# Optimization experiments

Measured on AMD Instinct MI355X. Metric: run time of the kernel, lower is better.

Reference implementation:

```python
import jax, jax.numpy as jnp
import numpy as np

N = 100000       # nodes per graph
H = 384          # hidden_dim
GRID = 10 * 10 * 7   # flattened grid feature size (10x10 UV grid, 7 channels)
NTYPES = 6       # len(surface_type_map)
ENT = NTYPES + 1 # one-hot entity_types + scalar area


def setup_inputs() -> dict:
    key = jax.random.key(0)
    ks = jax.random.split(key, 16)
    f32 = jnp.float32
    d = {}
    d["x1"] = jax.random.normal(ks[0], (N, 10, 10, 7), dtype=f32)
    d["is_face1"] = jax.random.uniform(ks[1], (N,), dtype=f32)
    d["entity_types1"] = jax.random.randint(ks[2], (N,), 0, NTYPES)
    d["area1"] = jax.random.uniform(ks[3], (N,), dtype=f32)
    d["x2"] = jax.random.normal(ks[4], (N, 10, 10, 7), dtype=f32)
    d["is_face2"] = jax.random.uniform(ks[5], (N,), dtype=f32)
    d["entity_types2"] = jax.random.randint(ks[6], (N,), 0, NTYPES)
    d["area2"] = jax.random.uniform(ks[7], (N,), dtype=f32)
    # MLP params (num_layers=2: Linear -> ELU -> Linear), fan-in scaled init
    d["W1g"] = jax.random.normal(ks[8], (GRID, H), dtype=f32) / np.sqrt(GRID)
    d["b1g"] = jnp.zeros((H,), dtype=f32)
    d["W2g"] = jax.random.normal(ks[9], (H, H), dtype=f32) / np.sqrt(H)
    d["b2g"] = jnp.zeros((H,), dtype=f32)
    d["W1e"] = jax.random.normal(ks[10], (ENT, H), dtype=f32) / np.sqrt(ENT)
    d["b1e"] = jnp.zeros((H,), dtype=f32)
    d["W2e"] = jax.random.normal(ks[11], (H, H), dtype=f32) / np.sqrt(H)
    d["b2e"] = jnp.zeros((H,), dtype=f32)
    return d


def _embed_one(x, is_face, entity_types, area, W1g, b1g, W2g, b2g, W1e, b1e, W2e, b2e):
    n = x.shape[0]
    face_mask = is_face > 0.5                      # which nodes are B-rep faces
    grid = x.reshape(n, -1)                        # [n, 700], mlp path
    hg = jax.nn.elu(grid @ W1g + b1g) @ W2g + b2g  # grid branch MLP
    ent = jnp.concatenate(
        [jax.nn.one_hot(entity_types, NTYPES, dtype=x.dtype), area[:, None]], axis=1
    )                                              # [n, 7]
    he = jax.nn.elu(ent @ W1e + b1e) @ W2e + b2e   # entity branch MLP
    # gather->MLP->scatter-add into zeros == masked dense (no batchnorm, row-wise MLP)
    return jnp.where(face_mask[:, None], hg + he, jnp.zeros((), x.dtype))


def reference(x1, is_face1, entity_types1, area1, x2, is_face2, entity_types2, area2,
              W1g, b1g, W2g, b2g, W1e, b1e, W2e, b2e):
    o1 = _embed_one(x1, is_face1, entity_types1, area1, W1g, b1g, W2g, b2g, W1e, b1e, W2e, b2e)
    o2 = _embed_one(x2, is_face2, entity_types2, area2, W1g, b1g, W2g, b2g, W1e, b1e, W2e, b2e)
    return (o1, o2)
```

## Files before the change

kernel.cpp:

```cpp
#include <hip/hip_runtime.h>
#include <hip/hip_bf16.h>

typedef __attribute__((ext_vector_type(8))) short short8;
typedef __attribute__((ext_vector_type(4))) short svec4;
typedef __attribute__((ext_vector_type(8))) __bf16 bf16x8;
typedef __attribute__((ext_vector_type(4))) float f32x4;

#define NN 100000
#define HD 384
#define K1T 22
#define K2T 24
#define NBLK 98

#define OFF_B1  0
#define OFF_B2  540672
#define OFF_T   1130496
#define OFF_V   1139712
#define OFF_BI  1141248
#define OFF_IDX 1142784
#define OFF_CNT 1942784
#define OFF_OFFS 1943568
#define OFF_TOT 1944352

union Frag { short s[8]; bf16x8 v; };

__device__ __forceinline__ short f2bf(float f) {
  union { __bf16 h; short s; } u;
  u.h = (__bf16)f;
  return u.s;
}

__device__ __forceinline__ float elu(float v) {
  return v > 0.f ? v : __expf(v) - 1.f;
}

__global__ void prep_kernel(const float* __restrict__ W1g, const float* __restrict__ b1g,
                            const float* __restrict__ W2g, const float* __restrict__ b2g,
                            const float* __restrict__ W1e, const float* __restrict__ b1e,
                            const float* __restrict__ W2e, const float* __restrict__ b2e,
                            char* __restrict__ ws) {
  int t = blockIdx.x * 256 + threadIdx.x;
  short* B1 = (short*)(ws + OFF_B1);
  short* B2 = (short*)(ws + OFF_B2);
  float* Tt = (float*)(ws + OFF_T);
  float* Vt = (float*)(ws + OFF_V);
  float* Bi = (float*)(ws + OFF_BI);
  if (t < 33792) {
    int lane = t & 63, rest = t >> 6;
    int kt = rest % K1T, nt = rest / K1T;
    int col = nt * 16 + (lane & 15);
    int kb = kt * 32 + (lane >> 4) * 8;
    short8 v;
#pragma unroll
    for (int i = 0; i < 8; ++i) {
      int k = kb + i;
      v[i] = (k < 700) ? f2bf(W1g[k * 384 + col]) : (short)0;
    }
    *(short8*)(B1 + (size_t)t * 8) = v;
  } else if (t < 70656) {
    int t2 = t - 33792;
    int lane = t2 & 63, rest = t2 >> 6;
    int kt = rest % K2T, nt = rest / K2T;
    int col = nt * 16 + (lane & 15);
    int kb = kt * 32 + (lane >> 4) * 8;
    short8 v;
#pragma unroll
    for (int i = 0; i < 8; ++i) {
      int k = kb + i;
      v[i] = (k < 384) ? f2bf(W2g[k * 384 + col]) : f2bf(W2e[(k - 384) * 384 + col]);
    }
    *(short8*)(B2 + (size_t)t2 * 8) = v;
  } else if (t < 73728) {
    int r = t - 70656;
    int which = r / 384, c = r % 384;
    if (which < 6)       Tt[r] = W1e[which * 384 + c] + b1e[c];
    else if (which == 6) Vt[c] = W1e[6 * 384 + c];
    else                 Bi[c] = b2g[c] + b2e[c];
  }
}

__global__ void count_kernel(const float* __restrict__ isf1, const float* __restrict__ isf2,
                             char* __restrict__ ws) {
  int g = blockIdx.y;
  const float* isf = g ? isf2 : isf1;
  int i = blockIdx.x * 1024 + threadIdx.x;
  bool face = (i < NN) && (isf[i] > 0.5f);
  unsigned long long b = __ballot(face);
  __shared__ int wc[16];
  int lane = threadIdx.x & 63, wid = threadIdx.x >> 6;
  if (lane == 0) wc[wid] = __popcll(b);
  __syncthreads();
  if (threadIdx.x == 0) {
    int s = 0;
#pragma unroll
    for (int w = 0; w < 16; ++w) s += wc[w];
    ((int*)(ws + OFF_CNT))[g * NBLK + blockIdx.x] = s;
  }
}

__global__ void scan_kernel(char* __restrict__ ws) {
  int t = threadIdx.x;
  if (t < 2) {
    const int* cnt = (const int*)(ws + OFF_CNT) + t * NBLK;
    int* offs = (int*)(ws + OFF_OFFS) + t * NBLK;
    int* tot = (int*)(ws + OFF_TOT);
    int run = 0;
    for (int b = 0; b < NBLK; ++b) { offs[b] = run; run += cnt[b]; }
    tot[t] = run;
  }
}

__global__ void compact_kernel(const float* __restrict__ isf1, const float* __restrict__ isf2,
                               char* __restrict__ ws) {
  int g = blockIdx.y;
  const float* isf = g ? isf2 : isf1;
  const int* offs = (const int*)(ws + OFF_OFFS) + g * NBLK;
  int totF = ((const int*)(ws + OFF_TOT))[g];
  int* idx = (int*)(ws + OFF_IDX) + g * NN;
  int bx = blockIdx.x;
  int i = bx * 1024 + threadIdx.x;
  bool valid = i < NN;
  bool face = valid && (isf[i] > 0.5f);
  unsigned long long bf = __ballot(face);
  unsigned long long bv = __ballot(valid);
  int lane = threadIdx.x & 63, wid = threadIdx.x >> 6;
  __shared__ int wF[16], wV[16];
  if (lane == 0) { wF[wid] = __popcll(bf); wV[wid] = __popcll(bv); }
  __syncthreads();
  int baseF = 0, baseV = 0;
  for (int w = 0; w < wid; ++w) { baseF += wF[w]; baseV += wV[w]; }
  unsigned long long lmask = (1ull << lane) - 1ull;
  int pF = __popcll(bf & lmask);
  int pV = __popcll(bv & lmask);
  if (face) {
    idx[offs[bx] + baseF + pF] = i;
  } else if (valid) {
    int nfBefore = bx * 1024 - offs[bx];
    int nfIn = (baseV + pV) - (baseF + pF);
    idx[totF + nfBefore + nfIn] = i;
  }
}

__global__ __launch_bounds__(256, 3) void face_embed_kernel(
    const float* __restrict__ x1, const int* __restrict__ et1, const float* __restrict__ ar1,
    const float* __restrict__ x2, const int* __restrict__ et2, const float* __restrict__ ar2,
    const float* __restrict__ b1g, const char* __restrict__ ws,
    float* __restrict__ out) {
  const int g = blockIdx.y;
  const float* x = g ? x2 : x1;
  const int* et  = g ? et2 : et1;
  const float* ar = g ? ar2 : ar1;
  float* o = out + (size_t)g * NN * HD;
  const int* idx = (const int*)(ws + OFF_IDX) + g * NN;
  const int totF = ((const int*)(ws + OFF_TOT))[g];
  const int nFB = (totF + 31) >> 5;
  const int bx = blockIdx.x;
  const int tid = threadIdx.x;

  if (bx >= nFB) {
    int totN = NN - totF;
    int base = (bx - nFB) * 32;
    if (base >= totN) return;
    const int* idxN = idx + totF;
    f32x4 z = {0.f, 0.f, 0.f, 0.f};
#pragma unroll
    for (int it = 0; it < 12; ++it) {
      int c = tid + it * 256;
      int r = c / 96, cc = c % 96;
      if (base + r < totN) {
        int node = idxN[base + r];
        *(f32x4*)(o + (size_t)node * HD + cc * 4) = z;
      }
    }
    return;
  }

  __shared__ short As[32 * 704];
  __shared__ int sN[32];
  short* h1s = As;

  const bf16x8* B1 = (const bf16x8*)(ws + OFF_B1);
  const bf16x8* B2 = (const bf16x8*)(ws + OFF_B2);
  const float* Tg  = (const float*)(ws + OFF_T);
  const float* Vg  = (const float*)(ws + OFF_V);
  const float* Big = (const float*)(ws + OFF_BI);

  const int row0 = bx * 32;
  if (tid < 32) {
    sN[tid] = (row0 + tid < totF) ? idx[row0 + tid] : -1;
    int byte = (tid * 1408 + 1400) ^ ((tid & 7) << 4);
    *(unsigned long long*)((char*)As + byte) = 0ull;
  }
  __syncthreads();

#pragma unroll 4
  for (int it = 0; it < 22; ++it) {
    int c = tid + it * 256;
    if (c < 5600) {
      int r = c / 175, cc = c % 175;
      int node = sN[r];
      if (node >= 0) {
        f32x4 v = *(const f32x4*)(x + (size_t)node * 700 + cc * 4);
        svec4 p;
#pragma unroll
        for (int i = 0; i < 4; ++i) p[i] = f2bf(v[i]);
        int byte = (r * 1408 + cc * 8) ^ ((r & 7) << 4);
        *(svec4*)((char*)As + byte) = p;
      }
    }
  }

  const int wid = tid >> 6, lane = tid & 63;
  const int lr = lane & 15, gq = lane >> 4;

  float b1c[6], b2c[6];
#pragma unroll
  for (int n = 0; n < 6; ++n) {
    int col = (wid * 6 + n) * 16 + lr;
    b1c[n] = b1g[col];
    b2c[n] = Big[col];
  }
  __syncthreads();

  f32x4 acc[2][6] = {};
  for (int kt = 0; kt < K1T; ++kt) {
    Frag a[2];
#pragma unroll
    for (int m = 0; m < 2; ++m) {
      int row = m * 16 + lr;
      int byte = (row * 1408 + kt * 64 + gq * 16) ^ ((row & 7) << 4);
      a[m].v = *(const bf16x8*)((const char*)As + byte);
    }
#pragma unroll
    for (int n = 0; n < 6; ++n) {
      bf16x8 b = B1[((wid * 6 + n) * K1T + kt) * 64 + lane];
#pragma unroll
      for (int m = 0; m < 2; ++m)
        acc[m][n] = __builtin_amdgcn_mfma_f32_16x16x32_bf16(a[m].v, b, acc[m][n], 0, 0, 0);
    }
  }
  __syncthreads();

#pragma unroll
  for (int m = 0; m < 2; ++m)
#pragma unroll
    for (int n = 0; n < 6; ++n) {
      int col = (wid * 6 + n) * 16 + lr;
#pragma unroll
      for (int r2 = 0; r2 < 4; ++r2) {
        int row = m * 16 + 4 * gq + r2;
        float hv = elu(acc[m][n][r2] + b1c[n]);
        int byte = (row * 768 + col * 2) ^ ((row & 15) << 4);
        *(short*)((char*)h1s + byte) = f2bf(hv);
      }
    }
  __syncthreads();

  int nde[2]; float nda[2];
#pragma unroll
  for (int m = 0; m < 2; ++m) {
    int node = sN[m * 16 + lr];
    if (node >= 0) { nde[m] = et[node]; nda[m] = ar[node]; }
    else           { nde[m] = 0;        nda[m] = 0.f; }
  }

  f32x4 acc2[2][6] = {};
  for (int kt = 0; kt < K2T; ++kt) {
    Frag a[2];
    if (kt < 12) {
#pragma unroll
      for (int m = 0; m < 2; ++m) {
        int row = m * 16 + lr;
        int byte = (row * 768 + (kt * 32 + gq * 8) * 2) ^ ((row & 15) << 4);
        a[m].v = *(const bf16x8*)((const char*)h1s + byte);
      }
    } else {
      int c0 = (kt - 12) * 32 + gq * 8;
#pragma unroll
      for (int m = 0; m < 2; ++m) {
        const float* Tp = Tg + nde[m] * 384 + c0;
        const float* Vp = Vg + c0;
#pragma unroll
        for (int i = 0; i < 8; ++i)
          a[m].s[i] = f2bf(elu(Tp[i] + nda[m] * Vp[i]));
      }
    }
#pragma unroll
    for (int n = 0; n < 6; ++n) {
      bf16x8 b = B2[((wid * 6 + n) * K2T + kt) * 64 + lane];
#pragma unroll
      for (int m = 0; m < 2; ++m)
        acc2[m][n] = __builtin_amdgcn_mfma_f32_16x16x32_bf16(a[m].v, b, acc2[m][n], 0, 0, 0);
    }
  }

#pragma unroll
  for (int m = 0; m < 2; ++m) {
#pragma unroll
    for (int r2 = 0; r2 < 4; ++r2) {
      int node = sN[m * 16 + 4 * gq + r2];
      if (node >= 0) {
#pragma unroll
        for (int n = 0; n < 6; ++n) {
          int col = (wid * 6 + n) * 16 + lr;
          o[(size_t)node * HD + col] = acc2[m][n][r2] + b2c[n];
        }
      }
    }
  }
}

extern "C" void kernel_launch(void* const* d_in, const int* in_sizes, int n_in,
                              void* d_out, int out_size, void* d_ws, size_t ws_size,
                              hipStream_t stream) {
  (void)n_in; (void)out_size; (void)ws_size; (void)in_sizes;
  const float* x1  = (const float*)d_in[0];
  const float* is1 = (const float*)d_in[1];
  const int*   et1 = (const int*)d_in[2];
  const float* ar1 = (const float*)d_in[3];
  const float* x2  = (const float*)d_in[4];
  const float* is2 = (const float*)d_in[5];
  const int*   et2 = (const int*)d_in[6];
  const float* ar2 = (const float*)d_in[7];
  const float* W1g = (const float*)d_in[8];
  const float* b1g = (const float*)d_in[9];
  const float* W2g = (const float*)d_in[10];
  const float* b2g = (const float*)d_in[11];
  const float* W1e = (const float*)d_in[12];
  const float* b1e = (const float*)d_in[13];
  const float* W2e = (const float*)d_in[14];
  const float* b2e = (const float*)d_in[15];
  float* out = (float*)d_out;
  char* ws = (char*)d_ws;

  prep_kernel<<<dim3(288), dim3(256), 0, stream>>>(W1g, b1g, W2g, b2g, W1e, b1e, W2e, b2e, ws);
  count_kernel<<<dim3(NBLK, 2), dim3(1024), 0, stream>>>(is1, is2, ws);
  scan_kernel<<<dim3(1), dim3(64), 0, stream>>>(ws);
  compact_kernel<<<dim3(NBLK, 2), dim3(1024), 0, stream>>>(is1, is2, ws);

  dim3 grid(NN / 32 + 1, 2);
  face_embed_kernel<<<grid, dim3(256), 0, stream>>>(
      x1, et1, ar1, x2, et2, ar2, b1g, ws, out);
}
```

Before: 371.1 us.

## Load grid MFMA A-fragments directly from global, dropping LDS staging

The first GEMM no longer stages gathered x rows into shared memory. Each lane reads its A fragment straight from global memory, converts it to bf16 in registers, and zero-pads the tail of the 700-wide row. This removes the LDS tile, a staging loop and one barrier, shrinks shared memory (which may raise occupancy), and reuses one accumulator set for both GEMMs. In exchange, each wave issues redundant, less-coalesced global loads, and every wave re-reads the same A rows across its 6 column groups.

```diff
diff --git a/kernel.cpp b/kernel.cpp
--- a/kernel.cpp
+++ b/kernel.cpp
@@ -175,9 +175,8 @@
     return;
   }
 
-  __shared__ short As[32 * 704];
+  __shared__ short h1s[32 * 384];
   __shared__ int sN[32];
-  short* h1s = As;
 
   const bf16x8* B1 = (const bf16x8*)(ws + OFF_B1);
   const bf16x8* B2 = (const bf16x8*)(ws + OFF_B2);
@@ -186,29 +185,8 @@
   const float* Big = (const float*)(ws + OFF_BI);
 
   const int row0 = bx * 32;
-  if (tid < 32) {
-    sN[tid] = (row0 + tid < totF) ? idx[row0 + tid] : -1;
-    int byte = (tid * 1408 + 1400) ^ ((tid & 7) << 4);
-    *(unsigned long long*)((char*)As + byte) = 0ull;
-  }
+  if (tid < 32) sN[tid] = (row0 + tid < totF) ? idx[row0 + tid] : -1;
   __syncthreads();
-
-#pragma unroll 4
-  for (int it = 0; it < 22; ++it) {
-    int c = tid + it * 256;
-    if (c < 5600) {
-      int r = c / 175, cc = c % 175;
-      int node = sN[r];
-      if (node >= 0) {
-        f32x4 v = *(const f32x4*)(x + (size_t)node * 700 + cc * 4);
-        svec4 p;
-#pragma unroll
-        for (int i = 0; i < 4; ++i) p[i] = f2bf(v[i]);
-        int byte = (r * 1408 + cc * 8) ^ ((r & 7) << 4);
-        *(svec4*)((char*)As + byte) = p;
-      }
-    }
-  }
 
   const int wid = tid >> 6, lane = tid & 63;
   const int lr = lane & 15, gq = lane >> 4;
@@ -220,16 +198,30 @@
     b1c[n] = b1g[col];
     b2c[n] = Big[col];
   }
-  __syncthreads();
+  int nde[2]; float nda[2];
+  const float* xp[2];
+#pragma unroll
+  for (int m = 0; m < 2; ++m) {
+    int node = sN[m * 16 + lr];
+    if (node >= 0) { nde[m] = et[node]; nda[m] = ar[node]; }
+    else           { nde[m] = 0;        nda[m] = 0.f; node = sN[0]; }
+    xp[m] = x + (size_t)node * 700;
+  }
 
   f32x4 acc[2][6] = {};
+
   for (int kt = 0; kt < K1T; ++kt) {
+    int k0 = kt * 32 + gq * 8;
     Frag a[2];
 #pragma unroll
     for (int m = 0; m < 2; ++m) {
-      int row = m * 16 + lr;
-      int byte = (row * 1408 + kt * 64 + gq * 16) ^ ((row & 7) << 4);
-      a[m].v = *(const bf16x8*)((const char*)As + byte);
+      const float* p = xp[m] + k0;
+      f32x4 lo = *(const f32x4*)p;
+      f32x4 hi;
+      if (kt == 21 && gq == 3) hi = (f32x4){0.f, 0.f, 0.f, 0.f};
+      else                     hi = *(const f32x4*)(p + 4);
+#pragma unroll
+      for (int i = 0; i < 4; ++i) { a[m].s[i] = f2bf(lo[i]); a[m].s[4 + i] = f2bf(hi[i]); }
     }
 #pragma unroll
     for (int n = 0; n < 6; ++n) {
@@ -239,7 +231,6 @@
         acc[m][n] = __builtin_amdgcn_mfma_f32_16x16x32_bf16(a[m].v, b, acc[m][n], 0, 0, 0);
     }
   }
-  __syncthreads();
 
 #pragma unroll
   for (int m = 0; m < 2; ++m)
@@ -256,15 +247,12 @@
     }
   __syncthreads();
 
-  int nde[2]; float nda[2];
-#pragma unroll
-  for (int m = 0; m < 2; ++m) {
-    int node = sN[m * 16 + lr];
-    if (node >= 0) { nde[m] = et[node]; nda[m] = ar[node]; }
-    else           { nde[m] = 0;        nda[m] = 0.f; }
-  }
-
-  f32x4 acc2[2][6] = {};
+#pragma unroll
+  for (int m = 0; m < 2; ++m)
+#pragma unroll
+    for (int n = 0; n < 6; ++n)
+      acc[m][n] = (f32x4){0.f, 0.f, 0.f, 0.f};
+
   for (int kt = 0; kt < K2T; ++kt) {
     Frag a[2];
     if (kt < 12) {
@@ -290,7 +278,7 @@
       bf16x8 b = B2[((wid * 6 + n) * K2T + kt) * 64 + lane];
 #pragma unroll
       for (int m = 0; m < 2; ++m)
-        acc2[m][n] = __builtin_amdgcn_mfma_f32_16x16x32_bf16(a[m].v, b, acc2[m][n], 0, 0, 0);
+        acc[m][n] = __builtin_amdgcn_mfma_f32_16x16x32_bf16(a[m].v, b, acc[m][n], 0, 0, 0);
     }
   }
 
@@ -303,7 +291,7 @@
 #pragma unroll
         for (int n = 0; n < 6; ++n) {
           int col = (wid * 6 + n) * 16 + lr;
-          o[(size_t)node * HD + col] = acc2[m][n][r2] + b2c[n];
+          o[(size_t)node * HD + col] = acc[m][n][r2] + b2c[n];
         }
       }
     }
```

After: 400.3 us. +7.9%, slower.
